# Optimization experiments

Hardware: AMD Instinct MI355X
Metric: run time of the kernel (lower is better)

The kernel has to match this reference:

```python
import jax, jax.numpy as jnp
import numpy as np


def _silu(v):
    return v * jax.nn.sigmoid(v)


def setup_inputs() -> dict:
    key = jax.random.key(0)
    ks = jax.random.split(key, 12)
    B, N, DS = 4, 12500, 63      # batch, nodes per graph, dim_single
    E = 800000                   # total edges (avg degree 16)
    BN = B * N
    ND = DS + 1                  # node_dim = dim_single + 1 (timestep channel)
    H, ED = 128, 32              # hidden_dim, edge_dim (fixed in __init__)
    MIN = 2 * ND + ED            # m_input feature dim = 160

    def lin(k, i, o):
        return (jax.random.normal(k, (i, o)) / np.sqrt(i)).astype(jnp.float32)

    return {
        "x": jax.random.normal(ks[0], (B, N, 3), dtype=jnp.float32) * 5.0,
        "cond": jax.random.normal(ks[1], (B, N, DS), dtype=jnp.float32),
        "edge_dist": jax.random.uniform(ks[2], (E,), dtype=jnp.float32) * 15.0,
        "ew1": lin(ks[3], 1, ED), "eb1": jnp.zeros((ED,), jnp.float32),
        "ew2": lin(ks[4], ED, ED), "eb2": jnp.zeros((ED,), jnp.float32),
        "nw1": lin(ks[5], MIN, H), "nb1": jnp.zeros((H,), jnp.float32),
        "nw2": lin(ks[6], H, ND), "nb2": jnp.zeros((ND,), jnp.float32),
        "cw1": lin(ks[7], MIN, H), "cb1": jnp.zeros((H,), jnp.float32),
        "cw2": lin(ks[8], H, 1),
        "edge_index": jax.random.randint(ks[9], (2, E), 0, BN, dtype=jnp.int64 if jax.config.jax_enable_x64 else jnp.int32),
        "t": 100,
    }


def reference(x, cond, edge_dist, ew1, eb1, ew2, eb2, nw1, nb1, nw2, nb2,
              cw1, cb1, cw2, edge_index, t):
    B, N, _ = x.shape
    BN = B * N
    # append timestep scalar channel to conditioning -> node features h
    t_feat = jnp.full((B, N, 1), t, dtype=x.dtype)
    h = jnp.concatenate([cond, t_feat], axis=-1).reshape(BN, -1)   # [BN, node_dim]
    xf = x.reshape(BN, 3)

    src, dst = edge_index[0], edge_index[1]
    # edge_mlp on scalar distances -> [E, edge_dim]
    edge_attr = _silu(edge_dist[:, None] @ ew1 + eb1) @ ew2 + eb2
    # gather + concat -> [E, 2*node_dim + edge_dim]
    m_input = jnp.concatenate([h[src], h[dst], edge_attr], axis=-1)
    # node_mlp (its output h_agg is discarded by p_sample, kept for faithfulness)
    m = _silu(m_input @ nw1 + nb1) @ nw2 + nb2
    h_agg = jax.ops.segment_sum(m, dst, num_segments=BN)
    h_out = h + h_agg  # unused by p_sample's return
    del h_out
    # coord_mlp -> scalar weight per edge
    coord_weight = _silu(m_input @ cw1 + cb1) @ cw2                 # [E, 1]
    dir_vec = xf[src] - xf[dst]                                     # [E, 3]
    dir_len = jnp.maximum(jnp.linalg.norm(dir_vec, axis=-1, keepdims=True), 1e-8)
    coord_update = coord_weight * (dir_vec / dir_len)
    x_agg = jax.ops.segment_sum(coord_update, dst, num_segments=BN)
    return (xf + x_agg).reshape(B, N, 3)
```

## Files before the change

### kernel.cpp

```cpp
#include <hip/hip_runtime.h>
#include <hip/hip_bf16.h>

typedef __attribute__((ext_vector_type(8))) short bf16x8;
typedef __attribute__((ext_vector_type(4))) float f32x4;
typedef __attribute__((ext_vector_type(4), aligned(4))) float f32x4u;
typedef __attribute__((ext_vector_type(2), aligned(4))) float f32x2u;

__device__ __forceinline__ unsigned short f2bf(float f) {
    unsigned int u = __float_as_uint(f);
    unsigned int r = (u + 0x7fffu + ((u >> 16) & 1u)) >> 16;
    return (unsigned short)r;
}
__device__ __forceinline__ float bflo(unsigned int u) { return __uint_as_float(u << 16); }
__device__ __forceinline__ float bfhi(unsigned int u) { return __uint_as_float(u & 0xffff0000u); }

__device__ __forceinline__ bf16x8 load8_bf(const float* p) {
    f32x4u a = *(const f32x4u*)p;
    f32x4u b = *(const f32x4u*)(p + 4);
    bf16x8 r;
    r[0] = f2bf(a[0]); r[1] = f2bf(a[1]); r[2] = f2bf(a[2]); r[3] = f2bf(a[3]);
    r[4] = f2bf(b[0]); r[5] = f2bf(b[1]); r[6] = f2bf(b[2]); r[7] = f2bf(b[3]);
    return r;
}
__device__ __forceinline__ bf16x8 load7z_bf(const float* p) {
    f32x4u a = *(const f32x4u*)p;
    f32x2u b = *(const f32x2u*)(p + 4);
    float c = p[6];
    bf16x8 r;
    r[0] = f2bf(a[0]); r[1] = f2bf(a[1]); r[2] = f2bf(a[2]); r[3] = f2bf(a[3]);
    r[4] = f2bf(b[0]); r[5] = f2bf(b[1]); r[6] = f2bf(c);  r[7] = 0;
    return r;
}

__global__ __launch_bounds__(256) void prep_kernel(
    const float* __restrict__ x, float* __restrict__ out, int n_out,
    const float* __restrict__ cond, const float* __restrict__ cw1,
    const float* __restrict__ ew2, const float* __restrict__ eb2,
    const float* __restrict__ cb1, const int* __restrict__ tptr,
    unsigned short* __restrict__ bt_M, float* __restrict__ c0,
    unsigned short* __restrict__ UV, int BN, int nb_uv)
{
    const int b = blockIdx.x, tid = threadIdx.x;
    if (b < nb_uv) {
        __shared__ __align__(16) unsigned short bt2[256 * 72];
        {
            const int c = tid;
            const float* colp = (c < 128) ? (cw1 + c) : (cw1 + 64 * 128 + (c - 128));
            for (int k = 0; k < 63; ++k)
                bt2[c * 72 + k] = f2bf(colp[k * 128]);
            bt2[c * 72 + 63] = 0;
        }
        __syncthreads();

        const int lane = tid & 63, wid = tid >> 6;
        const int fr = lane & 15, kq = lane >> 4;
        int node = b * 64 + wid * 16 + fr;
        if (node >= BN) node = BN - 1;
        const float* cp = cond + (long)node * 63;
        bf16x8 b0 = load8_bf(cp + 8 * kq);
        bf16x8 b1 = (kq < 3) ? load8_bf(cp + 32 + 8 * kq) : load7z_bf(cp + 56);

        char* UVb = (char*)UV;
        const unsigned off0 = (unsigned)node * 512u + (unsigned)(kq * 8);
        #pragma unroll
        for (int n = 0; n < 16; ++n) {
            bf16x8 a0 = *reinterpret_cast<const bf16x8*>(&bt2[(n * 16 + fr) * 72 + 8 * kq]);
            bf16x8 a1 = *reinterpret_cast<const bf16x8*>(&bt2[(n * 16 + fr) * 72 + 32 + 8 * kq]);
            f32x4 acc = (f32x4){0.f, 0.f, 0.f, 0.f};
            acc = __builtin_amdgcn_mfma_f32_16x16x32_bf16(a0, b0, acc, 0, 0, 0);
            acc = __builtin_amdgcn_mfma_f32_16x16x32_bf16(a1, b1, acc, 0, 0, 0);
            uint2 pk;
            pk.x = (unsigned)f2bf(acc[0]) | ((unsigned)f2bf(acc[1]) << 16);
            pk.y = (unsigned)f2bf(acc[2]) | ((unsigned)f2bf(acc[3]) << 16);
            *reinterpret_cast<uint2*>(UVb + off0 + n * 32) = pk;
        }
    } else if (b == nb_uv) {
        if (tid < 128) {
            int j = tid;
            float t = (float)tptr[0];
            float cacc = cb1[j] + t * (cw1[63 * 128 + j] + cw1[127 * 128 + j]);
            float m[32];
            #pragma unroll
            for (int p = 0; p < 32; ++p) m[p] = 0.f;
            for (int i = 0; i < 32; ++i) {
                float w = cw1[(128 + i) * 128 + j];
                cacc = fmaf(eb2[i], w, cacc);
                #pragma unroll
                for (int p = 0; p < 32; ++p) m[p] = fmaf(ew2[p * 32 + i], w, m[p]);
            }
            c0[j] = cacc;
            #pragma unroll
            for (int p = 0; p < 32; ++p) bt_M[j * 32 + p] = f2bf(m[p]);
        }
    } else {
        int i = (b - nb_uv - 1) * 256 + tid;
        if (i < n_out) out[i] = x[i];
    }
}

__global__ __launch_bounds__(256, 4) void edge_kernel(
    const float* __restrict__ x, const float* __restrict__ edge_dist,
    const float* __restrict__ ew1, const float* __restrict__ eb1,
    const unsigned short* __restrict__ bt_M, const float* __restrict__ c0f,
    const float* __restrict__ cw2, const unsigned short* __restrict__ UV,
    const int* __restrict__ edge_index, float* __restrict__ out, int E)
{
    __shared__ __align__(16) unsigned short s_lds[128][40];
    __shared__ int idx_lds[2][128];
    __shared__ float cw_lds[128];

    const int tid = threadIdx.x, lane = tid & 63, wid = tid >> 6;
    const int fr = lane & 15, kq = lane >> 4;
    const int lp = lane & 31, hf = lane >> 5;
    const int e0w = blockIdx.x * 128 + wid * 32;

    {
        int e = e0w + lp; if (e >= E) e = E - 1;
        idx_lds[hf][wid * 32 + lp] = edge_index[hf ? (E + e) : e];
    }
    asm volatile("s_waitcnt lgkmcnt(0)" ::: "memory");
    int srow[2], drow[2];
    #pragma unroll
    for (int m = 0; m < 2; ++m) {
        srow[m] = idx_lds[0][wid * 32 + m * 16 + fr];
        drow[m] = idx_lds[1][wid * 32 + m * 16 + fr];
    }

    const char* UVb = (const char*)UV;
    uint2 Lu[2][8], Lv[2][8];
    #pragma unroll
    for (int m = 0; m < 2; ++m) {
        unsigned bu = (unsigned)srow[m] * 512u + (unsigned)(kq * 8);
        unsigned bv = (unsigned)drow[m] * 512u + 256u + (unsigned)(kq * 8);
        #pragma unroll
        for (int g = 0; g < 8; ++g) {
            Lu[m][g] = *reinterpret_cast<const uint2*>(UVb + bu + g * 32);
            Lv[m][g] = *reinterpret_cast<const uint2*>(UVb + bv + g * 32);
        }
    }

    {
        int eh = lane >> 1, j0 = (lane & 1) * 16;
        int e = e0w + eh; if (e >= E) e = E - 1;
        float dist = edge_dist[e];
        f32x4u wv[4], bb[4];
        #pragma unroll
        for (int i = 0; i < 4; ++i) {
            wv[i] = *reinterpret_cast<const f32x4u*>(ew1 + j0 + 4 * i);
            bb[i] = *reinterpret_cast<const f32x4u*>(eb1 + j0 + 4 * i);
        }
        unsigned pk[8];
        #pragma unroll
        for (int i = 0; i < 8; ++i) {
            float a0 = fmaf(dist, wv[i >> 1][(i & 1) * 2 + 0], bb[i >> 1][(i & 1) * 2 + 0]);
            float a1 = fmaf(dist, wv[i >> 1][(i & 1) * 2 + 1], bb[i >> 1][(i & 1) * 2 + 1]);
            float s0 = a0 / (1.f + __expf(-a0));
            float s1 = a1 / (1.f + __expf(-a1));
            pk[i] = (unsigned)f2bf(s0) | ((unsigned)f2bf(s1) << 16);
        }
        uint4 q0 = make_uint4(pk[0], pk[1], pk[2], pk[3]);
        uint4 q1 = make_uint4(pk[4], pk[5], pk[6], pk[7]);
        *reinterpret_cast<uint4*>(&s_lds[wid * 32 + eh][j0]) = q0;
        *reinterpret_cast<uint4*>(&s_lds[wid * 32 + eh][j0 + 8]) = q1;
    }
    asm volatile("s_waitcnt lgkmcnt(0)" ::: "memory");

    bf16x8 sb[2];
    #pragma unroll
    for (int m = 0; m < 2; ++m)
        sb[m] = *reinterpret_cast<const bf16x8*>(&s_lds[wid * 32 + m * 16 + fr][8 * kq]);

    float psum[2] = {0.f, 0.f};
    #pragma unroll
    for (int nh = 0; nh < 2; ++nh) {
        f32x4 acc[2][4];
        #pragma unroll
        for (int n = 0; n < 4; ++n) {
            const int g = nh * 4 + n;
            f32x4u c = *reinterpret_cast<const f32x4u*>(c0f + g * 16 + kq * 4);
            #pragma unroll
            for (int m = 0; m < 2; ++m) {
                unsigned u0 = Lu[m][g].x, u1 = Lu[m][g].y;
                unsigned v0 = Lv[m][g].x, v1 = Lv[m][g].y;
                acc[m][n] = (f32x4){ c[0] + bflo(u0) + bflo(v0),
                                     c[1] + bfhi(u0) + bfhi(v0),
                                     c[2] + bflo(u1) + bflo(v1),
                                     c[3] + bfhi(u1) + bfhi(v1) };
            }
        }
        #pragma unroll
        for (int n = 0; n < 4; ++n) {
            const int g = nh * 4 + n;
            bf16x8 aw = *reinterpret_cast<const bf16x8*>(&bt_M[(g * 16 + fr) * 32 + 8 * kq]);
            acc[0][n] = __builtin_amdgcn_mfma_f32_16x16x32_bf16(aw, sb[0], acc[0][n], 0, 0, 0);
            acc[1][n] = __builtin_amdgcn_mfma_f32_16x16x32_bf16(aw, sb[1], acc[1][n], 0, 0, 0);
        }
        #pragma unroll
        for (int n = 0; n < 4; ++n) {
            const int g = nh * 4 + n;
            f32x4u w2 = *reinterpret_cast<const f32x4u*>(cw2 + g * 16 + kq * 4);
            #pragma unroll
            for (int m = 0; m < 2; ++m)
                #pragma unroll
                for (int r = 0; r < 4; ++r) {
                    float h = acc[m][n][r];
                    float sil = h / (1.f + __expf(-h));
                    psum[m] = fmaf(sil, w2[r], psum[m]);
                }
        }
    }

    #pragma unroll
    for (int m = 0; m < 2; ++m) {
        psum[m] += __shfl_xor(psum[m], 16, 64);
        psum[m] += __shfl_xor(psum[m], 32, 64);
    }
    if (kq == 0) {
        #pragma unroll
        for (int m = 0; m < 2; ++m)
            cw_lds[wid * 32 + m * 16 + fr] = psum[m];
    }
    asm volatile("s_waitcnt lgkmcnt(0)" ::: "memory");
    if (lane < 32) {
        int e = e0w + lp;
        if (e < E) {
            float coord_w = cw_lds[wid * 32 + lp];
            int src = idx_lds[0][wid * 32 + lp];
            int dst = idx_lds[1][wid * 32 + lp];
            float dx = x[src * 3 + 0] - x[dst * 3 + 0];
            float dy = x[src * 3 + 1] - x[dst * 3 + 1];
            float dz = x[src * 3 + 2] - x[dst * 3 + 2];
            float len = sqrtf(fmaf(dx, dx, fmaf(dy, dy, dz * dz)));
            len = fmaxf(len, 1e-8f);
            float sc = coord_w / len;
            atomicAdd(&out[dst * 3 + 0], sc * dx);
            atomicAdd(&out[dst * 3 + 1], sc * dy);
            atomicAdd(&out[dst * 3 + 2], sc * dz);
        }
    }
}

extern "C" void kernel_launch(void* const* d_in, const int* in_sizes, int n_in,
                              void* d_out, int out_size, void* d_ws, size_t ws_size,
                              hipStream_t stream) {
    const float* x         = (const float*)d_in[0];
    const float* cond      = (const float*)d_in[1];
    const float* edge_dist = (const float*)d_in[2];
    const float* ew1       = (const float*)d_in[3];
    const float* eb1       = (const float*)d_in[4];
    const float* ew2       = (const float*)d_in[5];
    const float* eb2       = (const float*)d_in[6];
    const float* cw1       = (const float*)d_in[11];
    const float* cb1       = (const float*)d_in[12];
    const float* cw2       = (const float*)d_in[13];
    const int*   edge_index= (const int*)d_in[14];
    const int*   tptr      = (const int*)d_in[15];
    float* out = (float*)d_out;

    const int E  = in_sizes[2];
    const int BN = in_sizes[1] / 63;
    const int n_out = out_size;

    char* ws = (char*)d_ws;
    unsigned short* bt_M = (unsigned short*)(ws);
    float*          c0   = (float*)(ws + 8192);
    unsigned short* UV   = (unsigned short*)(ws + 65536);

    const int nb_uv = (BN + 63) / 64;
    const int nb_out = (n_out + 255) / 256;
    prep_kernel<<<nb_uv + 1 + nb_out, 256, 0, stream>>>(
        x, out, n_out, cond, cw1, ew2, eb2, cb1, tptr, bt_M, c0, UV, BN, nb_uv);

    int blocks = (E + 127) / 128;
    edge_kernel<<<blocks, 256, 0, stream>>>(x, edge_dist, ew1, eb1,
                                            bt_M, c0, cw2, UV,
                                            edge_index, out, E);
}
```

Baseline: 271.5 us.

## Fuse prep and edge kernels into a persistent cooperative kernel with grid sync

Replaces the two-kernel sequence with a single cooperative persistent kernel. It copies x to the output, builds the per-node UV projections and the folded weights, then synchronises the whole grid and loops over edge tiles. The aim is to remove the second kernel launch and its tail. In exchange it pays for a grid-wide barrier, uses only occupancy-limited blocks (capped grid), and splits the UV projection into two halves to use less shared memory. The old two-kernel path stays as a fallback if the cooperative launch fails.

```diff
diff --git a/kernel.cpp b/kernel.cpp
--- a/kernel.cpp
+++ b/kernel.cpp
@@ -1,5 +1,8 @@
 #include <hip/hip_runtime.h>
 #include <hip/hip_bf16.h>
+#include <hip/hip_cooperative_groups.h>
+
+namespace cg = cooperative_groups;
 
 typedef __attribute__((ext_vector_type(8))) short bf16x8;
 typedef __attribute__((ext_vector_type(4))) float f32x4;
@@ -30,6 +33,231 @@
     r[0] = f2bf(a[0]); r[1] = f2bf(a[1]); r[2] = f2bf(a[2]); r[3] = f2bf(a[3]);
     r[4] = f2bf(b[0]); r[5] = f2bf(b[1]); r[6] = f2bf(c);  r[7] = 0;
     return r;
+}
+
+__global__ __launch_bounds__(256, 8) void fused_kernel(
+    const float* __restrict__ x, const float* __restrict__ cond,
+    const float* __restrict__ edge_dist,
+    const float* __restrict__ ew1, const float* __restrict__ eb1,
+    const float* __restrict__ ew2, const float* __restrict__ eb2,
+    const float* __restrict__ cw1, const float* __restrict__ cb1,
+    const float* __restrict__ cw2,
+    const int* __restrict__ edge_index, const int* __restrict__ tptr,
+    float* __restrict__ out,
+    unsigned short* __restrict__ bt_M, float* __restrict__ c0,
+    unsigned short* __restrict__ UV,
+    int E, int BN, int n_out)
+{
+    __shared__ __align__(16) unsigned short smem[128 * 72];
+
+    const int b = blockIdx.x, tid = threadIdx.x, ngrid = gridDim.x;
+    const int lane = tid & 63, wid = tid >> 6;
+    const int fr = lane & 15, kq = lane >> 4;
+
+    for (int i = b * 256 + tid; i < n_out; i += ngrid * 256)
+        out[i] = x[i];
+
+    if (b == 0) {
+        if (tid < 128) {
+            int j = tid;
+            float t = (float)tptr[0];
+            float cacc = cb1[j] + t * (cw1[63 * 128 + j] + cw1[127 * 128 + j]);
+            float m[32];
+            #pragma unroll
+            for (int p = 0; p < 32; ++p) m[p] = 0.f;
+            for (int i = 0; i < 32; ++i) {
+                float w = cw1[(128 + i) * 128 + j];
+                cacc = fmaf(eb2[i], w, cacc);
+                #pragma unroll
+                for (int p = 0; p < 32; ++p) m[p] = fmaf(ew2[p * 32 + i], w, m[p]);
+            }
+            c0[j] = cacc;
+            #pragma unroll
+            for (int p = 0; p < 32; ++p) bt_M[j * 32 + p] = f2bf(m[p]);
+        }
+    } else {
+        const int nuvb = ngrid - 1;
+        const int npb = (BN + nuvb - 1) / nuvb;
+        const int nbeg = (b - 1) * npb;
+        const int nend = (nbeg + npb < BN) ? (nbeg + npb) : BN;
+        if (nbeg < nend) {
+            for (int h = 0; h < 2; ++h) {
+                {
+                    const int c = tid >> 1;
+                    const float* colp = (h == 0) ? (cw1 + c) : (cw1 + 64 * 128 + c);
+                    const int k0 = (tid & 1) * 32;
+                    for (int kk = 0; kk < 32; ++kk) {
+                        int k = k0 + kk;
+                        float v = (k < 63) ? colp[k * 128] : 0.f;
+                        smem[c * 72 + k] = f2bf(v);
+                    }
+                }
+                __syncthreads();
+                for (int base = nbeg; base < nend; base += 64) {
+                    int node = base + wid * 16 + fr;
+                    if (node >= nend) node = nend - 1;
+                    const float* cp = cond + (long)node * 63;
+                    bf16x8 b0 = load8_bf(cp + 8 * kq);
+                    bf16x8 b1 = (kq < 3) ? load8_bf(cp + 32 + 8 * kq) : load7z_bf(cp + 56);
+                    char* UVb = (char*)UV;
+                    unsigned off0 = (unsigned)node * 512u + (unsigned)(h * 256) + (unsigned)(kq * 8);
+                    #pragma unroll
+                    for (int n = 0; n < 8; ++n) {
+                        bf16x8 a0 = *reinterpret_cast<const bf16x8*>(&smem[(n * 16 + fr) * 72 + 8 * kq]);
+                        bf16x8 a1 = *reinterpret_cast<const bf16x8*>(&smem[(n * 16 + fr) * 72 + 32 + 8 * kq]);
+                        f32x4 acc = (f32x4){0.f, 0.f, 0.f, 0.f};
+                        acc = __builtin_amdgcn_mfma_f32_16x16x32_bf16(a0, b0, acc, 0, 0, 0);
+                        acc = __builtin_amdgcn_mfma_f32_16x16x32_bf16(a1, b1, acc, 0, 0, 0);
+                        uint2 pk;
+                        pk.x = (unsigned)f2bf(acc[0]) | ((unsigned)f2bf(acc[1]) << 16);
+                        pk.y = (unsigned)f2bf(acc[2]) | ((unsigned)f2bf(acc[3]) << 16);
+                        *reinterpret_cast<uint2*>(UVb + off0 + n * 32) = pk;
+                    }
+                }
+                __syncthreads();
+            }
+        }
+    }
+
+    cg::this_grid().sync();
+
+    unsigned short (*s_lds)[40] = reinterpret_cast<unsigned short(*)[40]>(smem);
+    int*   idx0   = reinterpret_cast<int*>((char*)smem + 10240);
+    int*   idx1   = reinterpret_cast<int*>((char*)smem + 10752);
+    float* cw_lds = reinterpret_cast<float*>((char*)smem + 11264);
+
+    const int lp = lane & 31, hf = lane >> 5;
+    const int ntiles = (E + 127) / 128;
+    const char* UVb = (const char*)UV;
+
+    for (int t = b; t < ntiles; t += ngrid) {
+        const int e0w = t * 128 + wid * 32;
+
+        {
+            int e = e0w + lp; if (e >= E) e = E - 1;
+            int v = edge_index[hf ? (E + e) : e];
+            (hf ? idx1 : idx0)[wid * 32 + lp] = v;
+        }
+        asm volatile("s_waitcnt lgkmcnt(0)" ::: "memory");
+        int srow[2], drow[2];
+        #pragma unroll
+        for (int m = 0; m < 2; ++m) {
+            srow[m] = idx0[wid * 32 + m * 16 + fr];
+            drow[m] = idx1[wid * 32 + m * 16 + fr];
+        }
+
+        uint2 Lu[2][8], Lv[2][8];
+        #pragma unroll
+        for (int m = 0; m < 2; ++m) {
+            unsigned bu = (unsigned)srow[m] * 512u + (unsigned)(kq * 8);
+            unsigned bv = (unsigned)drow[m] * 512u + 256u + (unsigned)(kq * 8);
+            #pragma unroll
+            for (int g = 0; g < 8; ++g) {
+                Lu[m][g] = *reinterpret_cast<const uint2*>(UVb + bu + g * 32);
+                Lv[m][g] = *reinterpret_cast<const uint2*>(UVb + bv + g * 32);
+            }
+        }
+
+        {
+            int eh = lane >> 1, j0 = (lane & 1) * 16;
+            int e = e0w + eh; if (e >= E) e = E - 1;
+            float dist = edge_dist[e];
+            f32x4u wv[4], bb[4];
+            #pragma unroll
+            for (int i = 0; i < 4; ++i) {
+                wv[i] = *reinterpret_cast<const f32x4u*>(ew1 + j0 + 4 * i);
+                bb[i] = *reinterpret_cast<const f32x4u*>(eb1 + j0 + 4 * i);
+            }
+            unsigned pk[8];
+            #pragma unroll
+            for (int i = 0; i < 8; ++i) {
+                float a0 = fmaf(dist, wv[i >> 1][(i & 1) * 2 + 0], bb[i >> 1][(i & 1) * 2 + 0]);
+                float a1 = fmaf(dist, wv[i >> 1][(i & 1) * 2 + 1], bb[i >> 1][(i & 1) * 2 + 1]);
+                float s0 = a0 / (1.f + __expf(-a0));
+                float s1 = a1 / (1.f + __expf(-a1));
+                pk[i] = (unsigned)f2bf(s0) | ((unsigned)f2bf(s1) << 16);
+            }
+            uint4 q0 = make_uint4(pk[0], pk[1], pk[2], pk[3]);
+            uint4 q1 = make_uint4(pk[4], pk[5], pk[6], pk[7]);
+            *reinterpret_cast<uint4*>(&s_lds[wid * 32 + eh][j0]) = q0;
+            *reinterpret_cast<uint4*>(&s_lds[wid * 32 + eh][j0 + 8]) = q1;
+        }
+        asm volatile("s_waitcnt lgkmcnt(0)" ::: "memory");
+
+        bf16x8 sb[2];
+        #pragma unroll
+        for (int m = 0; m < 2; ++m)
+            sb[m] = *reinterpret_cast<const bf16x8*>(&s_lds[wid * 32 + m * 16 + fr][8 * kq]);
+
+        float psum[2] = {0.f, 0.f};
+        #pragma unroll
+        for (int nh = 0; nh < 2; ++nh) {
+            f32x4 acc[2][4];
+            #pragma unroll
+            for (int n = 0; n < 4; ++n) {
+                const int g = nh * 4 + n;
+                f32x4u c = *reinterpret_cast<const f32x4u*>(c0 + g * 16 + kq * 4);
+                #pragma unroll
+                for (int m = 0; m < 2; ++m) {
+                    unsigned u0 = Lu[m][g].x, u1 = Lu[m][g].y;
+                    unsigned v0 = Lv[m][g].x, v1 = Lv[m][g].y;
+                    acc[m][n] = (f32x4){ c[0] + bflo(u0) + bflo(v0),
+                                         c[1] + bfhi(u0) + bfhi(v0),
+                                         c[2] + bflo(u1) + bflo(v1),
+                                         c[3] + bfhi(u1) + bfhi(v1) };
+                }
+            }
+            #pragma unroll
+            for (int n = 0; n < 4; ++n) {
+                const int g = nh * 4 + n;
+                bf16x8 aw = *reinterpret_cast<const bf16x8*>(&bt_M[(g * 16 + fr) * 32 + 8 * kq]);
+                acc[0][n] = __builtin_amdgcn_mfma_f32_16x16x32_bf16(aw, sb[0], acc[0][n], 0, 0, 0);
+                acc[1][n] = __builtin_amdgcn_mfma_f32_16x16x32_bf16(aw, sb[1], acc[1][n], 0, 0, 0);
+            }
+            #pragma unroll
+            for (int n = 0; n < 4; ++n) {
+                const int g = nh * 4 + n;
+                f32x4u w2 = *reinterpret_cast<const f32x4u*>(cw2 + g * 16 + kq * 4);
+                #pragma unroll
+                for (int m = 0; m < 2; ++m)
+                    #pragma unroll
+                    for (int r = 0; r < 4; ++r) {
+                        float hh = acc[m][n][r];
+                        float sil = hh / (1.f + __expf(-hh));
+                        psum[m] = fmaf(sil, w2[r], psum[m]);
+                    }
+            }
+        }
+
+        #pragma unroll
+        for (int m = 0; m < 2; ++m) {
+            psum[m] += __shfl_xor(psum[m], 16, 64);
+            psum[m] += __shfl_xor(psum[m], 32, 64);
+        }
+        if (kq == 0) {
+            #pragma unroll
+            for (int m = 0; m < 2; ++m)
+                cw_lds[wid * 32 + m * 16 + fr] = psum[m];
+        }
+        asm volatile("s_waitcnt lgkmcnt(0)" ::: "memory");
+        if (lane < 32) {
+            int e = e0w + lp;
+            if (e < E) {
+                float coord_w = cw_lds[wid * 32 + lp];
+                int src = idx0[wid * 32 + lp];
+                int dst = idx1[wid * 32 + lp];
+                float dx = x[src * 3 + 0] - x[dst * 3 + 0];
+                float dy = x[src * 3 + 1] - x[dst * 3 + 1];
+                float dz = x[src * 3 + 2] - x[dst * 3 + 2];
+                float len = sqrtf(fmaf(dx, dx, fmaf(dy, dy, dz * dz)));
+                len = fmaxf(len, 1e-8f);
+                float sc = coord_w / len;
+                atomicAdd(&out[dst * 3 + 0], sc * dx);
+                atomicAdd(&out[dst * 3 + 1], sc * dy);
+                atomicAdd(&out[dst * 3 + 2], sc * dz);
+            }
+        }
+    }
 }
 
 __global__ __launch_bounds__(256) void prep_kernel(
@@ -51,7 +279,6 @@
             bt2[c * 72 + 63] = 0;
         }
         __syncthreads();
-
         const int lane = tid & 63, wid = tid >> 6;
         const int fr = lane & 15, kq = lane >> 4;
         int node = b * 64 + wid * 16 + fr;
@@ -59,7 +286,6 @@
         const float* cp = cond + (long)node * 63;
         bf16x8 b0 = load8_bf(cp + 8 * kq);
         bf16x8 b1 = (kq < 3) ? load8_bf(cp + 32 + 8 * kq) : load7z_bf(cp + 56);
-
         char* UVb = (char*)UV;
         const unsigned off0 = (unsigned)node * 512u + (unsigned)(kq * 8);
         #pragma unroll
@@ -125,7 +351,6 @@
         srow[m] = idx_lds[0][wid * 32 + m * 16 + fr];
         drow[m] = idx_lds[1][wid * 32 + m * 16 + fr];
     }
-
     const char* UVb = (const char*)UV;
     uint2 Lu[2][8], Lv[2][8];
     #pragma unroll
@@ -138,7 +363,6 @@
             Lv[m][g] = *reinterpret_cast<const uint2*>(UVb + bv + g * 32);
         }
     }
-
     {
         int eh = lane >> 1, j0 = (lane & 1) * 16;
         int e = e0w + eh; if (e >= E) e = E - 1;
@@ -164,12 +388,10 @@
         *reinterpret_cast<uint4*>(&s_lds[wid * 32 + eh][j0 + 8]) = q1;
     }
     asm volatile("s_waitcnt lgkmcnt(0)" ::: "memory");
-
     bf16x8 sb[2];
     #pragma unroll
     for (int m = 0; m < 2; ++m)
         sb[m] = *reinterpret_cast<const bf16x8*>(&s_lds[wid * 32 + m * 16 + fr][8 * kq]);
-
     float psum[2] = {0.f, 0.f};
     #pragma unroll
     for (int nh = 0; nh < 2; ++nh) {
@@ -209,7 +431,6 @@
                 }
         }
     }
-
     #pragma unroll
     for (int m = 0; m < 2; ++m) {
         psum[m] += __shfl_xor(psum[m], 16, 64);
@@ -266,13 +487,32 @@
     float*          c0   = (float*)(ws + 8192);
     unsigned short* UV   = (unsigned short*)(ws + 65536);
 
-    const int nb_uv = (BN + 63) / 64;
-    const int nb_out = (n_out + 255) / 256;
-    prep_kernel<<<nb_uv + 1 + nb_out, 256, 0, stream>>>(
-        x, out, n_out, cond, cw1, ew2, eb2, cb1, tptr, bt_M, c0, UV, BN, nb_uv);
-
-    int blocks = (E + 127) / 128;
-    edge_kernel<<<blocks, 256, 0, stream>>>(x, edge_dist, ew1, eb1,
-                                            bt_M, c0, cw2, UV,
-                                            edge_index, out, E);
-}
+    int nb_per_cu = 0;
+    hipError_t qe = hipOccupancyMaxActiveBlocksPerMultiprocessor(
+        &nb_per_cu, (const void*)fused_kernel, 256, 0);
+    if (qe != hipSuccess || nb_per_cu < 1) nb_per_cu = 1;
+    int grid = nb_per_cu * 256;
+    if (grid > 4096) grid = 4096;
+
+    void* args[] = {
+        (void*)&x, (void*)&cond, (void*)&edge_dist,
+        (void*)&ew1, (void*)&eb1, (void*)&ew2, (void*)&eb2,
+        (void*)&cw1, (void*)&cb1, (void*)&cw2,
+        (void*)&edge_index, (void*)&tptr, (void*)&out,
+        (void*)&bt_M, (void*)&c0, (void*)&UV,
+        (void*)&E, (void*)&BN, (void*)&n_out
+    };
+    hipError_t le = hipLaunchCooperativeKernel(
+        (const void*)fused_kernel, dim3(grid), dim3(256), args, 0, stream);
+
+    if (le != hipSuccess) {
+        const int nb_uv = (BN + 63) / 64;
+        const int nb_out = (n_out + 255) / 256;
+        prep_kernel<<<nb_uv + 1 + nb_out, 256, 0, stream>>>(
+            x, out, n_out, cond, cw1, ew2, eb2, cb1, tptr, bt_M, c0, UV, BN, nb_uv);
+        int blocks = (E + 127) / 128;
+        edge_kernel<<<blocks, 256, 0, stream>>>(x, edge_dist, ew1, eb1,
+                                                bt_M, c0, cw2, UV,
+                                                edge_index, out, E);
+    }
+}
```

After: 656.0 us. 2.42x slower.
